# Optimization experiments

Measured on AMD Instinct MI355X. Metric: run time of the kernel, lower is better.

Reference implementation:

```python
import jax, jax.numpy as jnp
import numpy as np

D_MODEL = 2048
D_INNER = 2 * D_MODEL      # expand=2
D_STATE = 16
D_CONV = 4
DT_RANK = D_MODEL // 16    # ceil(2048/16)=128
BATCH, SEQLEN = 2, 1024


def setup_inputs() -> dict:
    key = jax.random.key(0)
    ks = jax.random.split(key, 10)
    s = 0.02
    inp = {
        "hidden_states": jax.random.normal(ks[0], (BATCH, SEQLEN, D_MODEL), jnp.float32),
        "in_proj_w": jax.random.normal(ks[1], (2 * D_INNER, D_MODEL), jnp.float32) * s,
        "conv_w": jax.random.normal(ks[2], (D_INNER, D_CONV), jnp.float32) * s,
        "conv_b": jax.random.normal(ks[3], (D_INNER,), jnp.float32) * s,
        "x_proj_w": jax.random.normal(ks[4], (DT_RANK + 2 * D_STATE, D_INNER), jnp.float32) * s,
        "dt_proj_w": jax.random.normal(ks[5], (D_INNER, DT_RANK), jnp.float32) * s,
        "dt_proj_b": jax.random.normal(ks[6], (D_INNER,), jnp.float32) * 0.1,
        "A_log": jnp.log(jnp.tile(jnp.arange(1, D_STATE + 1, dtype=jnp.float32), (D_INNER, 1))),
        "D": jnp.ones((D_INNER,), jnp.float32),
        "out_proj_w": jax.random.normal(ks[7], (D_MODEL, D_INNER), jnp.float32) * s,
    }
    return inp


def _mamba_forward(hidden_states, in_proj_w, conv_w, conv_b, x_proj_w,
                   dt_proj_w, dt_proj_b, A_log, D, out_proj_w):
    B, L, _ = hidden_states.shape
    # input projection -> x, z  (each [B, L, D_INNER])
    xz = jnp.einsum('bld,ed->ble', hidden_states, in_proj_w)
    x, z = jnp.split(xz, 2, axis=-1)
    # causal depthwise conv1d (kernel D_CONV) + SiLU
    x_pad = jnp.pad(x, ((0, 0), (D_CONV - 1, 0), (0, 0)))
    windows = jnp.stack([x_pad[:, k:k + L, :] for k in range(D_CONV)], axis=-1)  # [B,L,D,K]
    x_conv = jnp.einsum('bldk,dk->bld', windows, conv_w) + conv_b
    x_act = jax.nn.silu(x_conv)
    # data-dependent SSM parameters
    x_dbl = jnp.einsum('bld,ed->ble', x_act, x_proj_w)
    dt, Bc, Cc = jnp.split(x_dbl, [DT_RANK, DT_RANK + D_STATE], axis=-1)
    dt = jax.nn.softplus(jnp.einsum('blr,dr->bld', dt, dt_proj_w) + dt_proj_b)  # [B,L,D_INNER]
    A = -jnp.exp(A_log)  # [D_INNER, D_STATE]

    # selective scan over time (carry h: [B, D_INNER, D_STATE])
    def step(h, inp):
        x_t, dt_t, B_t, C_t = inp  # [B,D],[B,D],[B,N],[B,N]
        dA = jnp.exp(dt_t[:, :, None] * A[None])          # [B,D,N]
        dBx = dt_t[:, :, None] * B_t[:, None, :] * x_t[:, :, None]
        h = h * dA + dBx
        y = jnp.einsum('bdn,bn->bd', h, C_t)
        return h, y

    xs = (x_act.transpose(1, 0, 2), dt.transpose(1, 0, 2),
          Bc.transpose(1, 0, 2), Cc.transpose(1, 0, 2))
    h0 = jnp.zeros((B, D_INNER, D_STATE), x_act.dtype)
    _, ys = jax.lax.scan(step, h0, xs)          # [L,B,D_INNER]
    y = ys.transpose(1, 0, 2) + x_act * D       # skip connection D*x
    y = y * jax.nn.silu(z)                      # gating
    return jnp.einsum('bld,md->blm', y, out_proj_w)


def reference(hidden_states, in_proj_w, conv_w, conv_b, x_proj_w,
              dt_proj_w, dt_proj_b, A_log, D, out_proj_w):
    return _mamba_forward(hidden_states, in_proj_w, conv_w, conv_b, x_proj_w,
                          dt_proj_w, dt_proj_b, A_log, D, out_proj_w)
```

## Files before the change

### kernel.cpp

```cpp
#include <hip/hip_runtime.h>
#include <cstdint>
#include <cstddef>

#define D_MODEL 2048
#define D_INNER 4096
#define D_IN2   8192
#define D_STATE 16
#define D_CONVK 4
#define DT_RANK 128
#define BATCH   2
#define SEQLEN  1024
#define BL      (BATCH*SEQLEN)
#define XDBL_N  (DT_RANK + 2*D_STATE)
#define XPW_NPAD 256
#define XPROJ_SPLITS 8

#define NCHUNK  16
#define LCHUNK  (SEQLEN/NCHUNK)
#define CHW     (BATCH*D_INNER*D_STATE)

#define NB_HID  2048
#define NB_IPW  8192
#define NB_XPW  320
#define NB_DTW  256
#define NB_OPW  4096

typedef short  s8v  __attribute__((ext_vector_type(8)));
typedef float  f4v  __attribute__((ext_vector_type(4)));

__device__ __forceinline__ float softplus_f(float v) {
    return (v > 20.f) ? v : log1pf(__expf(v));
}
__device__ __forceinline__ float silu_f(float v) {
    return v / (1.f + __expf(-v));
}
__device__ __forceinline__ float bf2f(short s) {
    return __uint_as_float(((uint32_t)(uint16_t)s) << 16);
}
__device__ __forceinline__ uint16_t f2bf(float f) {
    uint32_t u = __float_as_uint(f);
    return (uint16_t)((u + 0x7FFFu + ((u >> 16) & 1u)) >> 16);
}
__device__ __forceinline__ uint32_t packbf(float lo, float hi) {
    return ((uint32_t)f2bf(hi) << 16) | (uint32_t)f2bf(lo);
}
__device__ __forceinline__ float quad_sum(float p) {
    p += __int_as_float(__builtin_amdgcn_update_dpp(
            0, __float_as_int(p), 0xB1, 0xF, 0xF, true));
    p += __int_as_float(__builtin_amdgcn_update_dpp(
            0, __float_as_int(p), 0x4E, 0xF, 0xF, true));
    return p;
}

#define GLD16(gp, lp)                                                          \
    __builtin_amdgcn_global_load_lds(                                          \
        (const __attribute__((address_space(1))) void*)(gp),                   \
        (__attribute__((address_space(3))) void*)(lp), 16, 0, 0)

__global__ __launch_bounds__(256)
void cast_all_kernel(const float* __restrict__ s0, uint32_t* __restrict__ d0,
                     const float* __restrict__ s1, uint32_t* __restrict__ d1,
                     const float* __restrict__ s2, uint32_t* __restrict__ d2,
                     const float* __restrict__ s3, uint32_t* __restrict__ d3,
                     const float* __restrict__ s4, uint32_t* __restrict__ d4)
{
    int blk = blockIdx.x;
    const float* src; uint32_t* dst; int base;
    if      (blk < NB_HID)                              { src = s0; dst = d0; base = blk; }
    else if (blk < NB_HID + NB_IPW)                     { src = s1; dst = d1; base = blk - NB_HID; }
    else if (blk < NB_HID + NB_IPW + NB_XPW)            { src = s2; dst = d2; base = blk - NB_HID - NB_IPW; }
    else if (blk < NB_HID + NB_IPW + NB_XPW + NB_DTW)   { src = s3; dst = d3; base = blk - NB_HID - NB_IPW - NB_XPW; }
    else                                                { src = s4; dst = d4; base = blk - NB_HID - NB_IPW - NB_XPW - NB_DTW; }
    const int i = base * 256 + threadIdx.x;
    const float4 a = ((const float4*)src)[i * 2];
    const float4 b = ((const float4*)src)[i * 2 + 1];
    uint4 o;
    o.x = packbf(a.x, a.y); o.y = packbf(a.z, a.w);
    o.z = packbf(b.x, b.y); o.w = packbf(b.z, b.w);
    ((uint4*)dst)[i] = o;
}

template<int EPI>
__global__ __launch_bounds__(256)
void gemm_bf16_mfma(const short* __restrict__ A, int lda,
                    const short* __restrict__ W, int ldw,
                    const float* __restrict__ bias,
                    void* __restrict__ Cv, int ldc,
                    int M, int N, int K, int kchunk)
{
    __shared__ short sA[128 * 64];
    __shared__ short sW[128 * 64];

    const int tid = threadIdx.x;
    const int w   = tid >> 6;
    const int L   = tid & 63;
    const int bm  = blockIdx.y * 128;
    const int bn  = blockIdx.x * 128;
    const int k0  = blockIdx.z * kchunk;

    const int rsub = L >> 3;
    const int c8   = (((L & 7) - rsub) & 7) * 8;
    const short* Ag[4]; const short* Wg[4];
#pragma unroll
    for (int j = 0; j < 4; j++) {
        Ag[j] = A + (size_t)(bm + w * 32 + j * 8 + rsub) * lda + c8 + k0;
        Wg[j] = W + (size_t)(bn + w * 32 + j * 8 + rsub) * ldw + c8 + k0;
    }

    const int wm = (w >> 1) * 64;
    const int wn = (w & 1) * 64;
    const int cl = L & 15;
    const int qd = L >> 4;

    f4v acc[4][4];
#pragma unroll
    for (int i = 0; i < 4; i++)
#pragma unroll
        for (int j = 0; j < 4; j++) acc[i][j] = (f4v){0.f, 0.f, 0.f, 0.f};

    for (int k = 0; k < kchunk; k += 64) {
#pragma unroll
        for (int j = 0; j < 4; j++)
            GLD16(Ag[j] + k, &sA[(w * 32 + j * 8) * 64]);
#pragma unroll
        for (int j = 0; j < 4; j++)
            GLD16(Wg[j] + k, &sW[(w * 32 + j * 8) * 64]);
        __syncthreads();
#pragma unroll
        for (int kk = 0; kk < 2; kk++) {
            const int sl = ((kk * 4 + qd + cl) & 7) * 8;
            s8v a[4], b[4];
#pragma unroll
            for (int mt = 0; mt < 4; mt++)
                a[mt] = *(const s8v*)&sA[(wm + mt * 16 + cl) * 64 + sl];
#pragma unroll
            for (int nt = 0; nt < 4; nt++)
                b[nt] = *(const s8v*)&sW[(wn + nt * 16 + cl) * 64 + sl];
#pragma unroll
            for (int mt = 0; mt < 4; mt++)
#pragma unroll
                for (int nt = 0; nt < 4; nt++)
                    acc[mt][nt] = __builtin_amdgcn_mfma_f32_16x16x32_bf16(
                        a[mt], b[nt], acc[mt][nt], 0, 0, 0);
        }
        __syncthreads();
    }

    float* Cf = (float*)Cv + (size_t)blockIdx.z * M * ldc;
    short* Cs = (short*)Cv;
#pragma unroll
    for (int mt = 0; mt < 4; mt++) {
        const int row0 = bm + wm + mt * 16 + qd * 4;
#pragma unroll
        for (int nt = 0; nt < 4; nt++) {
            const int col = bn + wn + nt * 16 + cl;
#pragma unroll
            for (int r = 0; r < 4; r++) {
                float v = acc[mt][nt][r];
                if (EPI == 1) v = softplus_f(v + bias[col]);
                if (EPI == 2) Cs[(size_t)(row0 + r) * ldc + col] = (short)f2bf(v);
                else          Cf[(size_t)(row0 + r) * ldc + col] = v;
            }
        }
    }
}

__global__ __launch_bounds__(256)
void conv_silu_kernel(const short* __restrict__ xz_bf,
                      const float* __restrict__ cw,
                      const float* __restrict__ cb,
                      short* __restrict__ x_bf)
{
    const int idx = blockIdx.x * 256 + threadIdx.x;
    const int d  = idx & (D_INNER - 1);
    const int bl = idx >> 12;
    const int l  = bl & (SEQLEN - 1);
    const int b  = bl >> 10;
    const short* xb = xz_bf + (size_t)b * SEQLEN * D_IN2 + d;
    float acc = cb[d];
#pragma unroll
    for (int k = 0; k < D_CONVK; k++) {
        const int ll = l + k - (D_CONVK - 1);
        if (ll >= 0) acc = fmaf(bf2f(xb[(size_t)ll * D_IN2]), cw[d * D_CONVK + k], acc);
    }
    x_bf[idx] = (short)f2bf(silu_f(acc));
}

__global__ __launch_bounds__(256)
void reduce_xdbl_kernel(const float* __restrict__ P,
                        float* __restrict__ xf,
                        short* __restrict__ xb)
{
    const int idx = blockIdx.x * 256 + threadIdx.x;
    if (idx >= BL * XDBL_N) return;
    const int m = idx / XDBL_N;
    const int n = idx - m * XDBL_N;
    float s = 0.f;
#pragma unroll
    for (int z = 0; z < XPROJ_SPLITS; z++)
        s += P[(size_t)z * BL * XPW_NPAD + (size_t)m * XPW_NPAD + n];
    xf[idx] = s;
    xb[idx] = (short)f2bf(s);
}

__global__ __launch_bounds__(256)
void scan_phase1(const short* __restrict__ x_bf, const float* __restrict__ dt,
                 const float* __restrict__ xdbl, const float* __restrict__ A_log,
                 float* __restrict__ h_end, float* __restrict__ Pprod)
{
    const int c   = blockIdx.y;
    const int ch0 = blockIdx.x * 64;
    const int b   = ch0 >> 12;
    const int d0  = ch0 & (D_INNER - 1);
    const int tid = threadIdx.x;
    const int g   = tid >> 2;
    const int q   = tid & 3;
    const int d   = d0 + g;

    const float4 Al = *(const float4*)&A_log[(d << 4) + (q << 2)];
    float An[4] = {-__expf(Al.x), -__expf(Al.y), -__expf(Al.z), -__expf(Al.w)};
    float h[4]  = {0.f, 0.f, 0.f, 0.f};
    float Pp[4] = {1.f, 1.f, 1.f, 1.f};

    __shared__ float s_x [16][68];
    __shared__ float s_dt[16][68];
    __shared__ float s_B [16][20];

    const int lt  = tid >> 4;
    const int ld4 = (tid & 15) * 4;

    for (int sub = 0; sub < LCHUNK / 16; sub++) {
        const int l0 = c * LCHUNK + sub * 16;
        const size_t bl = (size_t)(b * SEQLEN + l0 + lt);
        __syncthreads();
        {
            const short4 sx = *(const short4*)&x_bf[bl * D_INNER + d0 + ld4];
            const float4 dv = *(const float4*)&dt[bl * D_INNER + d0 + ld4];
            *(float4*)&s_x [lt][ld4] =
                make_float4(bf2f(sx.x), bf2f(sx.y), bf2f(sx.z), bf2f(sx.w));
            *(float4*)&s_dt[lt][ld4] = dv;
            if (tid < 64) {
                const int t2 = tid >> 2, k = (tid & 3) * 4;
                const size_t bl2 = (size_t)(b * SEQLEN + l0 + t2);
                *(float4*)&s_B[t2][k] =
                    *(const float4*)&xdbl[bl2 * XDBL_N + DT_RANK + k];
            }
        }
        __syncthreads();
#pragma unroll
        for (int t = 0; t < 16; t++) {
            const float xv  = s_x [t][g];
            const float dtv = s_dt[t][g];
            const float4 Bq = *(const float4*)&s_B[t][q * 4];
            const float Bv[4] = {Bq.x, Bq.y, Bq.z, Bq.w};
            const float dtx = dtv * xv;
#pragma unroll
            for (int j = 0; j < 4; j++) {
                const float dA = __expf(dtv * An[j]);
                h[j]  = fmaf(h[j], dA, dtx * Bv[j]);
                Pp[j] *= dA;
            }
        }
    }
    const size_t i0 = (size_t)c * CHW + (((size_t)(b * D_INNER + d)) << 4) + (q << 2);
    *(float4*)&h_end[i0] = make_float4(h[0], h[1], h[2], h[3]);
    *(float4*)&Pprod[i0] = make_float4(Pp[0], Pp[1], Pp[2], Pp[3]);
}

__global__ __launch_bounds__(256)
void scan_phase2(const float* __restrict__ h_end, const float* __restrict__ P,
                 float* __restrict__ h_in)
{
    const int i = blockIdx.x * 256 + threadIdx.x;
    float carry = 0.f;
#pragma unroll
    for (int c = 0; c < NCHUNK; c++) {
        h_in[(size_t)c * CHW + i] = carry;
        if (c < NCHUNK - 1)
            carry = fmaf(P[(size_t)c * CHW + i], carry, h_end[(size_t)c * CHW + i]);
    }
}

__global__ __launch_bounds__(256)
void scan_phase3(const short* __restrict__ x_bf, short* __restrict__ y_bf,
                 const float* __restrict__ dt, const float* __restrict__ xdbl,
                 const short* __restrict__ xz_bf, const float* __restrict__ A_log,
                 const float* __restrict__ Dvec, const float* __restrict__ h_in)
{
    const int c   = blockIdx.y;
    const int ch0 = blockIdx.x * 64;
    const int b   = ch0 >> 12;
    const int d0  = ch0 & (D_INNER - 1);
    const int tid = threadIdx.x;
    const int g   = tid >> 2;
    const int q   = tid & 3;
    const int d   = d0 + g;

    const float4 Al = *(const float4*)&A_log[(d << 4) + (q << 2)];
    float An[4] = {-__expf(Al.x), -__expf(Al.y), -__expf(Al.z), -__expf(Al.w)};
    const float Dd = Dvec[d];
    const float4 h4 = *(const float4*)
        &h_in[(size_t)c * CHW + (((size_t)(b * D_INNER + d)) << 4) + (q << 2)];
    float h[4] = {h4.x, h4.y, h4.z, h4.w};

    __shared__ float s_x [16][68];
    __shared__ float s_dt[16][68];
    __shared__ float s_z [16][68];
    __shared__ float s_B [16][20];
    __shared__ float s_C [16][20];

    const int lt  = tid >> 4;
    const int ld4 = (tid & 15) * 4;

    for (int sub = 0; sub < LCHUNK / 16; sub++) {
        const int l0 = c * LCHUNK + sub * 16;
        const size_t bl = (size_t)(b * SEQLEN + l0 + lt);
        __syncthreads();
        {
            const short4 sx = *(const short4*)&x_bf[bl * D_INNER + d0 + ld4];
            const float4 dv = *(const float4*)&dt[bl * D_INNER + d0 + ld4];
            const short4 zv = *(const short4*)&xz_bf[bl * D_IN2 + D_INNER + d0 + ld4];
            *(float4*)&s_x [lt][ld4] =
                make_float4(bf2f(sx.x), bf2f(sx.y), bf2f(sx.z), bf2f(sx.w));
            *(float4*)&s_dt[lt][ld4] = dv;
            *(float4*)&s_z [lt][ld4] =
                make_float4(bf2f(zv.x), bf2f(zv.y), bf2f(zv.z), bf2f(zv.w));
            if (tid < 128) {
                const int t2 = (tid & 63) >> 2, k = (tid & 3) * 4;
                const size_t bl2 = (size_t)(b * SEQLEN + l0 + t2);
                const int off = (tid < 64) ? 0 : D_STATE;
                const float4 v =
                    *(const float4*)&xdbl[bl2 * XDBL_N + DT_RANK + off + k];
                if (tid < 64) *(float4*)&s_B[t2][k] = v;
                else          *(float4*)&s_C[t2][k] = v;
            }
        }
        __syncthreads();
        const size_t orow = (size_t)(b * SEQLEN + l0);
#pragma unroll
        for (int t = 0; t < 16; t++) {
            const float xv  = s_x [t][g];
            const float dtv = s_dt[t][g];
            const float4 Bq = *(const float4*)&s_B[t][q * 4];
            const float4 Cq = *(const float4*)&s_C[t][q * 4];
            const float Bv[4] = {Bq.x, Bq.y, Bq.z, Bq.w};
            const float Cv[4] = {Cq.x, Cq.y, Cq.z, Cq.w};
            const float dtx = dtv * xv;
            float p = 0.f;
#pragma unroll
            for (int j = 0; j < 4; j++) {
                const float dA = __expf(dtv * An[j]);
                h[j] = fmaf(h[j], dA, dtx * Bv[j]);
                p = fmaf(h[j], Cv[j], p);
            }
            p = quad_sum(p);
            if (q == 0) {
                const float yv = fmaf(xv, Dd, p) * silu_f(s_z[t][g]);
                y_bf[(orow + t) * D_INNER + d] = (short)f2bf(yv);
            }
        }
    }
}

extern "C" void kernel_launch(void* const* d_in, const int* in_sizes, int n_in,
                              void* d_out, int out_size, void* d_ws, size_t ws_size,
                              hipStream_t stream)
{
    const float* hidden     = (const float*)d_in[0];
    const float* in_proj_w  = (const float*)d_in[1];
    const float* conv_w     = (const float*)d_in[2];
    const float* conv_b     = (const float*)d_in[3];
    const float* x_proj_w   = (const float*)d_in[4];
    const float* dt_proj_w  = (const float*)d_in[5];
    const float* dt_proj_b  = (const float*)d_in[6];
    const float* A_log      = (const float*)d_in[7];
    const float* Dvec       = (const float*)d_in[8];
    const float* out_proj_w = (const float*)d_in[9];
    float* out = (float*)d_out;

    const size_t MB = 1ull << 20;
    char* ws = (char*)d_ws;
    short* xz_bf   = (short*)(ws);
    short* x_bf    = (short*)(ws + 32 * MB);
    short* ipw_bf  = (short*)(ws + 48 * MB);
    short* y_bf    = (short*)(ws + 48 * MB);
    float* h_end   = (float*)(ws + 64 * MB);
    float* Pbuf    = (float*)(ws + 72 * MB);
    short* hid_bf  = (short*)(ws + 80 * MB);
    float* h_in    = (float*)(ws + 80 * MB);
    short* opw_bf  = (short*)(ws + 88 * MB);
    float* P_part  = (float*)(ws + 104 * MB);
    float* dt_f32  = (float*)(ws + 104 * MB);
    short* xpw_bf  = (short*)(ws + 136 * MB);
    short* dtw_bf  = (short*)(ws + 138 * MB);
    float* xdbl_f  = (float*)(ws + 139 * MB);
    short* xdbl_bf = (short*)(ws + 139 * MB + 1310720);

    const dim3 blk(256);

    hipMemsetAsync(xpw_bf, 0, (size_t)XPW_NPAD * D_INNER * 2, stream);
    cast_all_kernel<<<dim3(NB_HID + NB_IPW + NB_XPW + NB_DTW + NB_OPW), blk, 0, stream>>>(
        hidden, (uint32_t*)hid_bf, in_proj_w, (uint32_t*)ipw_bf,
        x_proj_w, (uint32_t*)xpw_bf, dt_proj_w, (uint32_t*)dtw_bf,
        out_proj_w, (uint32_t*)opw_bf);

    gemm_bf16_mfma<2><<<dim3(D_IN2 / 128, BL / 128, 1), blk, 0, stream>>>(
        hid_bf, D_MODEL, ipw_bf, D_MODEL, nullptr, xz_bf, D_IN2,
        BL, D_IN2, D_MODEL, D_MODEL);

    conv_silu_kernel<<<dim3((BL * D_INNER) / 256), blk, 0, stream>>>(
        xz_bf, conv_w, conv_b, x_bf);

    gemm_bf16_mfma<0><<<dim3(XPW_NPAD / 128, BL / 128, XPROJ_SPLITS), blk, 0, stream>>>(
        x_bf, D_INNER, xpw_bf, D_INNER, nullptr, P_part, XPW_NPAD,
        BL, XPW_NPAD, D_INNER, D_INNER / XPROJ_SPLITS);
    reduce_xdbl_kernel<<<dim3((BL * XDBL_N + 255) / 256), blk, 0, stream>>>(
        P_part, xdbl_f, xdbl_bf);

    gemm_bf16_mfma<1><<<dim3(D_INNER / 128, BL / 128, 1), blk, 0, stream>>>(
        xdbl_bf, XDBL_N, dtw_bf, DT_RANK, dt_proj_b, dt_f32, D_INNER,
        BL, D_INNER, DT_RANK, DT_RANK);

    scan_phase1<<<dim3(BATCH * D_INNER / 64, NCHUNK - 1), blk, 0, stream>>>(
        x_bf, dt_f32, xdbl_f, A_log, h_end, Pbuf);
    scan_phase2<<<dim3(CHW / 256), blk, 0, stream>>>(h_end, Pbuf, h_in);
    scan_phase3<<<dim3(BATCH * D_INNER / 64, NCHUNK), blk, 0, stream>>>(
        x_bf, y_bf, dt_f32, xdbl_f, xz_bf, A_log, Dvec, h_in);

    gemm_bf16_mfma<0><<<dim3(D_MODEL / 128, BL / 128, 1), blk, 0, stream>>>(
        y_bf, D_INNER, opw_bf, D_INNER, nullptr, out, D_MODEL,
        BL, D_MODEL, D_INNER, D_INNER);
}
```

Measured before the change: 506.6 us.

## Fuse split-K reduction, dt cast, and scan carry propagation; drop extra launches

The x_proj split-K GEMM now accumulates straight into the xdbl buffer with atomicAdd, which replaces the partial-sum buffer and its reduce kernel. The xdbl buffer and the padding rows of the x_proj weight are zeroed inside the cast kernel instead of by a memset. A dedicated dt GEMM reads fp32 xdbl, converts it to bf16 while staging it in shared memory, and applies the softplus bias epilogue. scan_phase3 recomputes each chunk's starting state from h_end and Pbuf, which removes scan_phase2. Together this cuts kernel launches and intermediate memory traffic, at the cost of atomic contention, nondeterministic summation order, and redundant serial carry work in later scan chunks.

```diff
diff --git a/kernel.cpp b/kernel.cpp
--- a/kernel.cpp
+++ b/kernel.cpp
@@ -19,11 +19,13 @@
 #define LCHUNK  (SEQLEN/NCHUNK)
 #define CHW     (BATCH*D_INNER*D_STATE)
 
-#define NB_HID  2048
-#define NB_IPW  8192
-#define NB_XPW  320
-#define NB_DTW  256
-#define NB_OPW  4096
+#define NB_HID   2048
+#define NB_IPW   8192
+#define NB_XPW   320
+#define NB_XPWZ  192
+#define NB_DTW   256
+#define NB_OPW   4096
+#define NB_XDBLZ 320
 
 typedef short  s8v  __attribute__((ext_vector_type(8)));
 typedef float  f4v  __attribute__((ext_vector_type(4)));
@@ -62,16 +64,21 @@
                      const float* __restrict__ s1, uint32_t* __restrict__ d1,
                      const float* __restrict__ s2, uint32_t* __restrict__ d2,
                      const float* __restrict__ s3, uint32_t* __restrict__ d3,
-                     const float* __restrict__ s4, uint32_t* __restrict__ d4)
+                     const float* __restrict__ s4, uint32_t* __restrict__ d4,
+                     uint32_t* __restrict__ z0,
+                     uint32_t* __restrict__ z1)
 {
     int blk = blockIdx.x;
-    const float* src; uint32_t* dst; int base;
-    if      (blk < NB_HID)                              { src = s0; dst = d0; base = blk; }
-    else if (blk < NB_HID + NB_IPW)                     { src = s1; dst = d1; base = blk - NB_HID; }
-    else if (blk < NB_HID + NB_IPW + NB_XPW)            { src = s2; dst = d2; base = blk - NB_HID - NB_IPW; }
-    else if (blk < NB_HID + NB_IPW + NB_XPW + NB_DTW)   { src = s3; dst = d3; base = blk - NB_HID - NB_IPW - NB_XPW; }
-    else                                                { src = s4; dst = d4; base = blk - NB_HID - NB_IPW - NB_XPW - NB_DTW; }
+    const float* src = nullptr; uint32_t* dst; int base; int zero = 0;
+    if      (blk < NB_HID) { src = s0; dst = d0; base = blk; }
+    else if ((blk -= NB_HID)  < NB_IPW)  { src = s1; dst = d1; base = blk; }
+    else if ((blk -= NB_IPW)  < NB_XPW)  { src = s2; dst = d2; base = blk; }
+    else if ((blk -= NB_XPW)  < NB_XPWZ) { dst = z0; base = blk; zero = 1; }
+    else if ((blk -= NB_XPWZ) < NB_DTW)  { src = s3; dst = d3; base = blk; }
+    else if ((blk -= NB_DTW)  < NB_OPW)  { src = s4; dst = d4; base = blk; }
+    else                                 { dst = z1; base = blk - NB_OPW; zero = 1; }
     const int i = base * 256 + threadIdx.x;
+    if (zero) { ((uint4*)dst)[i] = make_uint4(0u, 0u, 0u, 0u); return; }
     const float4 a = ((const float4*)src)[i * 2];
     const float4 b = ((const float4*)src)[i * 2 + 1];
     uint4 o;
@@ -84,7 +91,6 @@
 __global__ __launch_bounds__(256)
 void gemm_bf16_mfma(const short* __restrict__ A, int lda,
                     const short* __restrict__ W, int ldw,
-                    const float* __restrict__ bias,
                     void* __restrict__ Cv, int ldc,
                     int M, int N, int K, int kchunk)
 {
@@ -146,7 +152,7 @@
         __syncthreads();
     }
 
-    float* Cf = (float*)Cv + (size_t)blockIdx.z * M * ldc;
+    float* Cf = (float*)Cv;
     short* Cs = (short*)Cv;
 #pragma unroll
     for (int mt = 0; mt < 4; mt++) {
@@ -154,13 +160,98 @@
 #pragma unroll
         for (int nt = 0; nt < 4; nt++) {
             const int col = bn + wn + nt * 16 + cl;
+            if (EPI == 3 && col >= XDBL_N) continue;
 #pragma unroll
             for (int r = 0; r < 4; r++) {
-                float v = acc[mt][nt][r];
-                if (EPI == 1) v = softplus_f(v + bias[col]);
-                if (EPI == 2) Cs[(size_t)(row0 + r) * ldc + col] = (short)f2bf(v);
-                else          Cf[(size_t)(row0 + r) * ldc + col] = v;
-            }
+                const float v = acc[mt][nt][r];
+                if      (EPI == 2) Cs[(size_t)(row0 + r) * ldc + col] = (short)f2bf(v);
+                else if (EPI == 3) atomicAdd(&Cf[(size_t)(row0 + r) * ldc + col], v);
+                else               Cf[(size_t)(row0 + r) * ldc + col] = v;
+            }
+        }
+    }
+}
+
+__global__ __launch_bounds__(256)
+void dt_gemm_kernel(const float* __restrict__ Af,
+                    const short* __restrict__ W,
+                    const float* __restrict__ bias,
+                    float* __restrict__ C)
+{
+    __shared__ short sA[2 * 128 * 64];
+    __shared__ short sW[2 * 128 * 64];
+
+    const int tid = threadIdx.x;
+    const int w   = tid >> 6;
+    const int L   = tid & 63;
+    const int bm  = blockIdx.y * 128;
+    const int bn  = blockIdx.x * 128;
+
+#pragma unroll
+    for (int ci = 0; ci < 8; ci++) {
+        const int c_lin = tid * 8 + ci;
+        const int r = c_lin >> 4;
+        const int c = c_lin & 15;
+        const float* src = Af + (size_t)(bm + r) * XDBL_N + c * 8;
+        const float4 u = *(const float4*)src;
+        const float4 v = *(const float4*)(src + 4);
+        const int half = c >> 3, cc = c & 7;
+        const int slot = (cc + r) & 7;
+        uint4 o;
+        o.x = packbf(u.x, u.y); o.y = packbf(u.z, u.w);
+        o.z = packbf(v.x, v.y); o.w = packbf(v.z, v.w);
+        *(uint4*)&sA[half * 8192 + r * 64 + slot * 8] = o;
+    }
+    const int rsub = L >> 3;
+    const int c8   = (((L & 7) - rsub) & 7) * 8;
+#pragma unroll
+    for (int half = 0; half < 2; half++)
+#pragma unroll
+        for (int j = 0; j < 4; j++)
+            GLD16(W + (size_t)(bn + w * 32 + j * 8 + rsub) * DT_RANK + half * 64 + c8,
+                  &sW[half * 8192 + (w * 32 + j * 8) * 64]);
+    __syncthreads();
+
+    const int wm = (w >> 1) * 64;
+    const int wn = (w & 1) * 64;
+    const int cl = L & 15;
+    const int qd = L >> 4;
+
+    f4v acc[4][4];
+#pragma unroll
+    for (int i = 0; i < 4; i++)
+#pragma unroll
+        for (int j = 0; j < 4; j++) acc[i][j] = (f4v){0.f, 0.f, 0.f, 0.f};
+
+#pragma unroll
+    for (int ks = 0; ks < 4; ks++) {
+        const int half = ks >> 1;
+        const int sl = (((ks & 1) * 4 + qd + cl) & 7) * 8;
+        s8v a[4], b[4];
+#pragma unroll
+        for (int mt = 0; mt < 4; mt++)
+            a[mt] = *(const s8v*)&sA[half * 8192 + (wm + mt * 16 + cl) * 64 + sl];
+#pragma unroll
+        for (int nt = 0; nt < 4; nt++)
+            b[nt] = *(const s8v*)&sW[half * 8192 + (wn + nt * 16 + cl) * 64 + sl];
+#pragma unroll
+        for (int mt = 0; mt < 4; mt++)
+#pragma unroll
+            for (int nt = 0; nt < 4; nt++)
+                acc[mt][nt] = __builtin_amdgcn_mfma_f32_16x16x32_bf16(
+                    a[mt], b[nt], acc[mt][nt], 0, 0, 0);
+    }
+
+#pragma unroll
+    for (int mt = 0; mt < 4; mt++) {
+        const int row0 = bm + wm + mt * 16 + qd * 4;
+#pragma unroll
+        for (int nt = 0; nt < 4; nt++) {
+            const int col = bn + wn + nt * 16 + cl;
+            const float bc = bias[col];
+#pragma unroll
+            for (int r = 0; r < 4; r++)
+                C[(size_t)(row0 + r) * D_INNER + col] = softplus_f(acc[mt][nt][r] + bc);
         }
     }
 }
@@ -184,23 +275,6 @@
         if (ll >= 0) acc = fmaf(bf2f(xb[(size_t)ll * D_IN2]), cw[d * D_CONVK + k], acc);
     }
     x_bf[idx] = (short)f2bf(silu_f(acc));
-}
-
-__global__ __launch_bounds__(256)
-void reduce_xdbl_kernel(const float* __restrict__ P,
-                        float* __restrict__ xf,
-                        short* __restrict__ xb)
-{
-    const int idx = blockIdx.x * 256 + threadIdx.x;
-    if (idx >= BL * XDBL_N) return;
-    const int m = idx / XDBL_N;
-    const int n = idx - m * XDBL_N;
-    float s = 0.f;
-#pragma unroll
-    for (int z = 0; z < XPROJ_SPLITS; z++)
-        s += P[(size_t)z * BL * XPW_NPAD + (size_t)m * XPW_NPAD + n];
-    xf[idx] = s;
-    xb[idx] = (short)f2bf(s);
 }
 
 __global__ __launch_bounds__(256)
@@ -268,24 +342,11 @@
 }
 
 __global__ __launch_bounds__(256)
-void scan_phase2(const float* __restrict__ h_end, const float* __restrict__ P,
-                 float* __restrict__ h_in)
-{
-    const int i = blockIdx.x * 256 + threadIdx.x;
-    float carry = 0.f;
-#pragma unroll
-    for (int c = 0; c < NCHUNK; c++) {
-        h_in[(size_t)c * CHW + i] = carry;
-        if (c < NCHUNK - 1)
-            carry = fmaf(P[(size_t)c * CHW + i], carry, h_end[(size_t)c * CHW + i]);
-    }
-}
-
-__global__ __launch_bounds__(256)
 void scan_phase3(const short* __restrict__ x_bf, short* __restrict__ y_bf,
                  const float* __restrict__ dt, const float* __restrict__ xdbl,
                  const short* __restrict__ xz_bf, const float* __restrict__ A_log,
-                 const float* __restrict__ Dvec, const float* __restrict__ h_in)
+                 const float* __restrict__ Dvec,
+                 const float* __restrict__ h_end, const float* __restrict__ Pbuf)
 {
     const int c   = blockIdx.y;
     const int ch0 = blockIdx.x * 64;
@@ -299,9 +360,17 @@
     const float4 Al = *(const float4*)&A_log[(d << 4) + (q << 2)];
     float An[4] = {-__expf(Al.x), -__expf(Al.y), -__expf(Al.z), -__expf(Al.w)};
     const float Dd = Dvec[d];
-    const float4 h4 = *(const float4*)
-        &h_in[(size_t)c * CHW + (((size_t)(b * D_INNER + d)) << 4) + (q << 2)];
-    float h[4] = {h4.x, h4.y, h4.z, h4.w};
+
+    float h[4] = {0.f, 0.f, 0.f, 0.f};
+    const size_t base = (((size_t)(b * D_INNER + d)) << 4) + (q << 2);
+    for (int j = 0; j < c; j++) {
+        const float4 he = *(const float4*)&h_end[(size_t)j * CHW + base];
+        const float4 Pp = *(const float4*)&Pbuf [(size_t)j * CHW + base];
+        h[0] = fmaf(Pp.x, h[0], he.x);
+        h[1] = fmaf(Pp.y, h[1], he.y);
+        h[2] = fmaf(Pp.z, h[2], he.z);
+        h[3] = fmaf(Pp.w, h[3], he.w);
+    }
 
     __shared__ float s_x [16][68];
     __shared__ float s_dt[16][68];
@@ -387,47 +456,42 @@
     float* h_end   = (float*)(ws + 64 * MB);
     float* Pbuf    = (float*)(ws + 72 * MB);
     short* hid_bf  = (short*)(ws + 80 * MB);
-    float* h_in    = (float*)(ws + 80 * MB);
     short* opw_bf  = (short*)(ws + 88 * MB);
-    float* P_part  = (float*)(ws + 104 * MB);
     float* dt_f32  = (float*)(ws + 104 * MB);
     short* xpw_bf  = (short*)(ws + 136 * MB);
     short* dtw_bf  = (short*)(ws + 138 * MB);
     float* xdbl_f  = (float*)(ws + 139 * MB);
-    short* xdbl_bf = (short*)(ws + 139 * MB + 1310720);
 
     const dim3 blk(256);
 
-    hipMemsetAsync(xpw_bf, 0, (size_t)XPW_NPAD * D_INNER * 2, stream);
-    cast_all_kernel<<<dim3(NB_HID + NB_IPW + NB_XPW + NB_DTW + NB_OPW), blk, 0, stream>>>(
+    cast_all_kernel<<<dim3(NB_HID + NB_IPW + NB_XPW + NB_XPWZ + NB_DTW + NB_OPW + NB_XDBLZ),
+                     blk, 0, stream>>>(
         hidden, (uint32_t*)hid_bf, in_proj_w, (uint32_t*)ipw_bf,
         x_proj_w, (uint32_t*)xpw_bf, dt_proj_w, (uint32_t*)dtw_bf,
-        out_proj_w, (uint32_t*)opw_bf);
+        out_proj_w, (uint32_t*)opw_bf,
+        (uint32_t*)(xpw_bf + (size_t)XDBL_N * D_INNER),
+        (uint32_t*)xdbl_f);
 
     gemm_bf16_mfma<2><<<dim3(D_IN2 / 128, BL / 128, 1), blk, 0, stream>>>(
-        hid_bf, D_MODEL, ipw_bf, D_MODEL, nullptr, xz_bf, D_IN2,
+        hid_bf, D_MODEL, ipw_bf, D_MODEL, xz_bf, D_IN2,
         BL, D_IN2, D_MODEL, D_MODEL);
 
     conv_silu_kernel<<<dim3((BL * D_INNER) / 256), blk, 0, stream>>>(
         xz_bf, conv_w, conv_b, x_bf);
 
-    gemm_bf16_mfma<0><<<dim3(XPW_NPAD / 128, BL / 128, XPROJ_SPLITS), blk, 0, stream>>>(
-        x_bf, D_INNER, xpw_bf, D_INNER, nullptr, P_part, XPW_NPAD,
+    gemm_bf16_mfma<3><<<dim3(XPW_NPAD / 128, BL / 128, XPROJ_SPLITS), blk, 0, stream>>>(
+        x_bf, D_INNER, xpw_bf, D_INNER, xdbl_f, XDBL_N,
         BL, XPW_NPAD, D_INNER, D_INNER / XPROJ_SPLITS);
-    reduce_xdbl_kernel<<<dim3((BL * XDBL_N + 255) / 256), blk, 0, stream>>>(
-        P_part, xdbl_f, xdbl_bf);
-
-    gemm_bf16_mfma<1><<<dim3(D_INNER / 128, BL / 128, 1), blk, 0, stream>>>(
-        xdbl_bf, XDBL_N, dtw_bf, DT_RANK, dt_proj_b, dt_f32, D_INNER,
-        BL, D_INNER, DT_RANK, DT_RANK);
+
+    dt_gemm_kernel<<<dim3(D_INNER / 128, BL / 128), blk, 0, stream>>>(
+        xdbl_f, dtw_bf, dt_proj_b, dt_f32);
 
     scan_phase1<<<dim3(BATCH * D_INNER / 64, NCHUNK - 1), blk, 0, stream>>>(
         x_bf, dt_f32, xdbl_f, A_log, h_end, Pbuf);
-    scan_phase2<<<dim3(CHW / 256), blk, 0, stream>>>(h_end, Pbuf, h_in);
     scan_phase3<<<dim3(BATCH * D_INNER / 64, NCHUNK), blk, 0, stream>>>(
-        x_bf, y_bf, dt_f32, xdbl_f, xz_bf, A_log, Dvec, h_in);
+        x_bf, y_bf, dt_f32, xdbl_f, xz_bf, A_log, Dvec, h_end, Pbuf);
 
     gemm_bf16_mfma<0><<<dim3(D_MODEL / 128, BL / 128, 1), blk, 0, stream>>>(
-        y_bf, D_INNER, opw_bf, D_INNER, nullptr, out, D_MODEL,
+        y_bf, D_INNER, opw_bf, D_INNER, out, D_MODEL,
         BL, D_MODEL, D_INNER, D_INNER);
 }
```

Result: faster. 483.4 us (-4.6%).
